# Performance work log

Measured on AMD Instinct MI355X. Metric: run time of the kernel, lower is better.

## Reference

```python
import jax, jax.numpy as jnp
import numpy as np

N_BASIS = 1024
KERNEL_SIZE = 1024
STRIDE = 256
N_BINS = N_BASIS // 2 + 1  # 513 (onesided)


def setup_inputs() -> dict:
    key = jax.random.key(0)
    x = jax.random.normal(key, (16, 1, 524288), dtype=jnp.float32)
    # omega = 2*pi*arange(n_basis//2+1)/n_basis (as in __init__)
    frequency = (2.0 * np.pi * jnp.arange(N_BINS, dtype=jnp.float32) / N_BASIS)
    # periodic hann window, matching torch.hann_window default
    n = jnp.arange(KERNEL_SIZE, dtype=jnp.float32)
    window = 0.5 * (1.0 - jnp.cos(2.0 * np.pi * n / KERNEL_SIZE))
    return {"x": x, "frequency": frequency, "window": window}


def _conv1d(x, kernel, stride):
    # x: (B, 1, T), kernel: (O, K) -> (B, O, F)
    return jax.lax.conv_general_dilated(
        x, kernel[:, None, :], window_strides=(stride,), padding="VALID",
        dimension_numbers=("NCH", "OIH", "NCH"))


def reference(x, frequency, window):
    # Fourier basis: cos(-omega*n), sin(-omega*n), windowed
    n = jnp.arange(KERNEL_SIZE, dtype=x.dtype)
    omega_n = frequency[:, None] * n[None, :]          # (513, K)
    basis_real = jnp.cos(-omega_n) * window            # (513, K)
    basis_imag = jnp.sin(-omega_n) * window            # (513, K)
    out_real = _conv1d(x, basis_real, STRIDE)          # (B, 513, F)
    out_imag = _conv1d(x, basis_imag, STRIDE)          # (B, 513, F)
    # return_complex=False: permute(0,3,1,2).view -> [real; imag] stacked on channels
    return jnp.concatenate([out_real, out_imag], axis=1)  # (B, 1026, F)
```

## Files before the change

### kernel.cpp

```cpp
#include <hip/hip_runtime.h>
#include <hip/hip_bf16.h>

#define TLEN   524288
#define NBATCH 16
#define KSZ    1024
#define NBINS  513
#define NCH    1026
#define NFRM   2045
#define HOP    256
#define MROWS  1024
#define KS2    512
#define NFPAD  2048
#define BM 128
#define BN 128
#define BK 64
#define NT 8
#define PREP_BASIS_BLKS 2048
#define PREP_FOLD_BLKS  8192

typedef __bf16 bf16x8 __attribute__((ext_vector_type(8)));
typedef float  f32x4  __attribute__((ext_vector_type(4)));
typedef unsigned short us8 __attribute__((ext_vector_type(8)));

__device__ __forceinline__ unsigned short f2b(float f) {
    return __builtin_bit_cast(unsigned short, __float2bfloat16(f));
}

__global__ void prep_k(const float* __restrict__ x,
                       const float* __restrict__ window,
                       __hip_bfloat16* __restrict__ basis,
                       __hip_bfloat16* __restrict__ u,
                       __hip_bfloat16* __restrict__ v,
                       float* __restrict__ out) {
    if (blockIdx.x < PREP_BASIS_BLKS) {
        int idx = blockIdx.x * 256 + threadIdx.x;
        int g = idx >> 9;
        int k = idx & (KS2 - 1);
        float val = 0.0f;
        if (g < 512) {
            if (k == 0) val = (g & 1) ? -1.0f : 1.0f;
            else {
                int m = (g * k) & (KSZ - 1);
                val = window[k] *
                      cosf((float)m * (6.283185307179586f / (float)KSZ));
            }
        } else if (g < 1023) {
            if (k != 0) {
                int c = g - 511;
                int m = (c * k) & (KSZ - 1);
                val = -window[k] *
                      sinf((float)m * (6.283185307179586f / (float)KSZ));
            }
        }
        basis[idx] = __float2bfloat16(val);
        return;
    }
    int idx = (blockIdx.x - PREP_BASIS_BLKS) * 256 + threadIdx.x;
    int b = idx >> 17;
    int rem = idx & ((1 << 17) - 1);
    int f = rem >> 6;
    int c = rem & 63;
    size_t orow = ((size_t)b * NFPAD + f) * KS2 + c * 8;
    us8 uo = {0, 0, 0, 0, 0, 0, 0, 0};
    us8 vo = {0, 0, 0, 0, 0, 0, 0, 0};
    float nacc = 0.0f;
    if (f < NFRM) {
        const float* xp = x + (size_t)b * TLEN + (size_t)f * HOP;
        float4 fw0 = *(const float4*)(xp + c * 8);
        float4 fw1 = *(const float4*)(xp + c * 8 + 4);
        float4 m0  = *(const float4*)(xp + 1016 - c * 8);
        float4 m1  = *(const float4*)(xp + 1020 - c * 8);
        float fwv[8] = {fw0.x, fw0.y, fw0.z, fw0.w,
                        fw1.x, fw1.y, fw1.z, fw1.w};
        float mv[9];
        mv[0] = m0.x; mv[1] = m0.y; mv[2] = m0.z; mv[3] = m0.w;
        mv[4] = m1.x; mv[5] = m1.y; mv[6] = m1.z; mv[7] = m1.w;
        mv[8] = (c > 0) ? xp[1024 - c * 8] : 0.0f;
        #pragma unroll
        for (int e = 0; e < 8; ++e) {
            float xf = fwv[e];
            float xm = mv[8 - e];
            float uval = xf + xm;
            uo[e] = f2b(uval);
            vo[e] = f2b(xf - xm);
            float wk = window[c * 8 + e];
            nacc += ((e & 1) ? -wk : wk) * uval;
        }
        if (c == 0) {
            float x512 = xp[512];
            uo[0] = f2b(x512);
            vo[0] = 0;
            nacc += x512;
        }
    }
    *(us8*)((unsigned short*)u + orow) = uo;
    *(us8*)((unsigned short*)v + orow) = vo;
    #pragma unroll
    for (int o = 32; o > 0; o >>= 1) nacc += __shfl_xor(nacc, o);
    if (f < NFRM) {
        if (c == 0) out[((size_t)b * NCH + 512) * NFRM + f] = nacc;
        if (c == 1) out[((size_t)b * NCH + 513) * NFRM + f] = 0.0f;
    }
}

__launch_bounds__(256, 2)
__global__ void stft_gemm_k(const __hip_bfloat16* __restrict__ basis,
                            const __hip_bfloat16* __restrict__ u,
                            const __hip_bfloat16* __restrict__ v,
                            float* __restrict__ out) {
    __shared__ __hip_bfloat16 As[BM * BK];
    __shared__ __hip_bfloat16 Bs[BN * BK];

    const int tid  = threadIdx.x;
    const int wave = tid >> 6;
    const int lane = tid & 63;
    const int l16  = lane & 15;
    const int lg   = lane >> 4;
    const int wr   = wave >> 1;
    const int wc   = wave & 1;
    const int f0   = blockIdx.x * BN;
    const int c0   = blockIdx.y * BM;
    const int bb   = blockIdx.z;
    const bool isV = (c0 >= 512);
    const __hip_bfloat16* Bmat =
        (isV ? v : u) + (size_t)bb * NFPAD * KS2;

    f32x4 acc[4][4] = {};

    for (int kt = 0; kt < NT; ++kt) {
        const int k0 = kt * BK;
        #pragma unroll
        for (int it = 0; it < 4; ++it) {
            int flat = it * 256 + tid;
            int row  = flat >> 3;
            int ch   = flat & 7;
            int kch  = ch ^ (row & 7);
            const __hip_bfloat16* sa =
                basis + (size_t)(c0 + row) * KS2 + k0 + kch * 8;
            __builtin_amdgcn_global_load_lds(
                (const __attribute__((address_space(1))) void*)sa,
                (__attribute__((address_space(3))) void*)
                    ((char*)As + (it * 256 + wave * 64) * 16),
                16, 0, 0);
            const __hip_bfloat16* sb =
                Bmat + (size_t)(f0 + row) * KS2 + k0 + kch * 8;
            __builtin_amdgcn_global_load_lds(
                (const __attribute__((address_space(1))) void*)sb,
                (__attribute__((address_space(3))) void*)
                    ((char*)Bs + (it * 256 + wave * 64) * 16),
                16, 0, 0);
        }
        __syncthreads();

        #pragma unroll
        for (int ks = 0; ks < 2; ++ks) {
            bf16x8 a[4], b[4];
            #pragma unroll
            for (int m = 0; m < 4; ++m) {
                int row  = wr * 64 + m * 16 + l16;
                int slot = row * 8 + ((ks * 4 + lg) ^ (row & 7));
                a[m] = *(const bf16x8*)((const char*)As + slot * 16);
            }
            #pragma unroll
            for (int n = 0; n < 4; ++n) {
                int row  = wc * 64 + n * 16 + l16;
                int slot = row * 8 + ((ks * 4 + lg) ^ (row & 7));
                b[n] = *(const bf16x8*)((const char*)Bs + slot * 16);
            }
            #pragma unroll
            for (int m = 0; m < 4; ++m)
                #pragma unroll
                for (int n = 0; n < 4; ++n)
                    acc[m][n] = __builtin_amdgcn_mfma_f32_16x16x32_bf16(
                        a[m], b[n], acc[m][n], 0, 0, 0);
        }
        __syncthreads();
    }

    const int choff = isV ? 2 : 0;
    float* outb = out + (size_t)bb * NCH * NFRM;
    #pragma unroll
    for (int m = 0; m < 4; ++m) {
        int g0 = c0 + wr * 64 + m * 16 + lg * 4;
        #pragma unroll
        for (int n = 0; n < 4; ++n) {
            int f = f0 + wc * 64 + n * 16 + l16;
            if (f < NFRM) {
                #pragma unroll
                for (int i = 0; i < 4; ++i)
                    outb[(size_t)(g0 + i + choff) * NFRM + f] = acc[m][n][i];
            }
        }
    }
}

extern "C" void kernel_launch(void* const* d_in, const int* in_sizes, int n_in,
                              void* d_out, int out_size, void* d_ws, size_t ws_size,
                              hipStream_t stream) {
    const float* x      = (const float*)d_in[0];
    const float* window = (const float*)d_in[2];

    __hip_bfloat16* basis = (__hip_bfloat16*)d_ws;
    __hip_bfloat16* ub = (__hip_bfloat16*)((char*)d_ws + (size_t)MROWS * KS2 * 2);
    __hip_bfloat16* vb = ub + (size_t)NBATCH * NFPAD * KS2;
    float* outp = (float*)d_out;

    prep_k<<<PREP_BASIS_BLKS + PREP_FOLD_BLKS, 256, 0, stream>>>(
        x, window, basis, ub, vb, outp);

    dim3 grid(NFPAD / BN, MROWS / BM, NBATCH);
    stft_gemm_k<<<grid, 256, 0, stream>>>(basis, ub, vb, outp);
}
```

Before: 72.54 us.

## Apply second-level even/odd frequency folding to halve GEMM reduction depth

Adds a further symmetry fold of each windowed frame: the 1024-tap window is split into quarter segments, and even/odd frequency bins get separate 256-deep basis planes, so the GEMM K dimension drops from 512 to 256. The prep kernel now applies the window to the input and writes four folded planes plus an x[512] side array. The GEMM epilogue scatters results to interleaved output channels with special-case corrections. This cuts MFMA work in half at the cost of a more complex prep, strided interleaved output writes, and extra bf16 rounding of windowed sums.

```diff
diff --git a/kernel.cpp b/kernel.cpp
--- a/kernel.cpp
+++ b/kernel.cpp
@@ -8,14 +8,15 @@
 #define NCH    1026
 #define NFRM   2045
 #define HOP    256
-#define MROWS  1024
-#define KS2    512
 #define NFPAD  2048
+#define KF     256
+#define M2     1024
+#define PS ((size_t)NBATCH * NFPAD * KF)
 #define BM 128
 #define BN 128
 #define BK 64
-#define NT 8
-#define PREP_BASIS_BLKS 2048
+#define NT 4
+#define PREP_BASIS_BLKS 1024
 #define PREP_FOLD_BLKS  8192
 
 typedef __bf16 bf16x8 __attribute__((ext_vector_type(8)));
@@ -29,84 +30,121 @@
 __global__ void prep_k(const float* __restrict__ x,
                        const float* __restrict__ window,
                        __hip_bfloat16* __restrict__ basis,
-                       __hip_bfloat16* __restrict__ u,
-                       __hip_bfloat16* __restrict__ v,
+                       __hip_bfloat16* __restrict__ planes,
+                       float* __restrict__ x512a,
                        float* __restrict__ out) {
     if (blockIdx.x < PREP_BASIS_BLKS) {
         int idx = blockIdx.x * 256 + threadIdx.x;
-        int g = idx >> 9;
-        int k = idx & (KS2 - 1);
+        int g = idx >> 8;
+        int k = idx & 255;
         float val = 0.0f;
-        if (g < 512) {
+        if (g < 256) {
             if (k == 0) val = (g & 1) ? -1.0f : 1.0f;
-            else {
-                int m = (g * k) & (KSZ - 1);
-                val = window[k] *
-                      cosf((float)m * (6.283185307179586f / (float)KSZ));
-            }
-        } else if (g < 1023) {
-            if (k != 0) {
-                int c = g - 511;
-                int m = (c * k) & (KSZ - 1);
-                val = -window[k] *
-                      sinf((float)m * (6.283185307179586f / (float)KSZ));
-            }
+            else { int m = (g * k) & 511;
+                   val = cosf((float)m * (6.283185307179586f / 512.0f)); }
+        } else if (g < 512) {
+            int d = g - 256, c = 2 * d + 1;
+            if (k) { int m = (c * k) & 1023;
+                     val = cosf((float)m * (6.283185307179586f / 1024.0f)); }
+        } else if (g < 768) {
+            int d = g - 512;
+            if (d <= 254 && k) {
+                int c = 2 * d + 2, m = (c * k) & 1023;
+                val = -sinf((float)m * (6.283185307179586f / 1024.0f));
+            }
+        } else {
+            int d = g - 768, c = 2 * d + 1;
+            if (k == 0) val = (d & 1) ? 1.0f : -1.0f;
+            else { int m = (c * k) & 1023;
+                   val = -sinf((float)m * (6.283185307179586f / 1024.0f)); }
         }
         basis[idx] = __float2bfloat16(val);
         return;
     }
-    int idx = (blockIdx.x - PREP_BASIS_BLKS) * 256 + threadIdx.x;
-    int b = idx >> 17;
-    int rem = idx & ((1 << 17) - 1);
-    int f = rem >> 6;
-    int c = rem & 63;
-    size_t orow = ((size_t)b * NFPAD + f) * KS2 + c * 8;
-    us8 uo = {0, 0, 0, 0, 0, 0, 0, 0};
-    us8 vo = {0, 0, 0, 0, 0, 0, 0, 0};
-    float nacc = 0.0f;
+    int wid  = (blockIdx.x - PREP_BASIS_BLKS) * 4 + (threadIdx.x >> 6);
+    int lane = threadIdx.x & 63;
+    int b = wid >> 11;
+    int f = wid & 2047;
+    int isQ = lane >> 5;
+    int j   = lane & 31;
+    size_t off = ((size_t)b * NFPAD + f) * KF + j * 8;
+    unsigned short* P0 = (unsigned short*)planes + (isQ ? 2 * PS : 0) + off;
+    unsigned short* P1 = (unsigned short*)planes + (isQ ? 3 * PS : PS) + off;
+    us8 o0 = {0, 0, 0, 0, 0, 0, 0, 0};
+    us8 o1 = {0, 0, 0, 0, 0, 0, 0, 0};
+    float nacc = 0.0f, x512 = 0.0f;
     if (f < NFRM) {
         const float* xp = x + (size_t)b * TLEN + (size_t)f * HOP;
-        float4 fw0 = *(const float4*)(xp + c * 8);
-        float4 fw1 = *(const float4*)(xp + c * 8 + 4);
-        float4 m0  = *(const float4*)(xp + 1016 - c * 8);
-        float4 m1  = *(const float4*)(xp + 1020 - c * 8);
-        float fwv[8] = {fw0.x, fw0.y, fw0.z, fw0.w,
-                        fw1.x, fw1.y, fw1.z, fw1.w};
-        float mv[9];
-        mv[0] = m0.x; mv[1] = m0.y; mv[2] = m0.z; mv[3] = m0.w;
-        mv[4] = m1.x; mv[5] = m1.y; mv[6] = m1.z; mv[7] = m1.w;
-        mv[8] = (c > 0) ? xp[1024 - c * 8] : 0.0f;
+        float4 a0 = *(const float4*)(xp + j * 8);
+        float4 a1 = *(const float4*)(xp + j * 8 + 4);
+        float4 r0 = *(const float4*)(xp + 1016 - j * 8);
+        float4 r1 = *(const float4*)(xp + 1020 - j * 8);
+        float4 cc0 = *(const float4*)(xp + 504 - j * 8);
+        float4 cc1 = *(const float4*)(xp + 508 - j * 8);
+        float4 d0 = *(const float4*)(xp + 512 + j * 8);
+        float4 d1 = *(const float4*)(xp + 512 + j * 8 + 4);
+        float4 w0 = *(const float4*)(window + j * 8);
+        float4 w1 = *(const float4*)(window + j * 8 + 4);
+        float4 wb0 = *(const float4*)(window + 504 - j * 8);
+        float4 wb1 = *(const float4*)(window + 508 - j * 8);
+        float S1 = (j > 0) ? xp[1024 - j * 8] : 0.0f;
+        float S2 = xp[512 - j * 8];
+        float SW = window[512 - j * 8];
+        float Av[8] = {a0.x, a0.y, a0.z, a0.w, a1.x, a1.y, a1.z, a1.w};
+        float Rv[8] = {r0.x, r0.y, r0.z, r0.w, r1.x, r1.y, r1.z, r1.w};
+        float Cv[8] = {cc0.x, cc0.y, cc0.z, cc0.w, cc1.x, cc1.y, cc1.z, cc1.w};
+        float Dv[8] = {d0.x, d0.y, d0.z, d0.w, d1.x, d1.y, d1.z, d1.w};
+        float Wa[8] = {w0.x, w0.y, w0.z, w0.w, w1.x, w1.y, w1.z, w1.w};
+        float Wb[8] = {wb0.x, wb0.y, wb0.z, wb0.w, wb1.x, wb1.y, wb1.z, wb1.w};
+        float p0slot = 0.0f;
         #pragma unroll
         for (int e = 0; e < 8; ++e) {
-            float xf = fwv[e];
-            float xm = mv[8 - e];
-            float uval = xf + xm;
-            uo[e] = f2b(uval);
-            vo[e] = f2b(xf - xm);
-            float wk = window[c * 8 + e];
-            nacc += ((e & 1) ? -wk : wk) * uval;
-        }
-        if (c == 0) {
-            float x512 = xp[512];
-            uo[0] = f2b(x512);
-            vo[0] = 0;
-            nacc += x512;
-        }
-    }
-    *(us8*)((unsigned short*)u + orow) = uo;
-    *(us8*)((unsigned short*)v + orow) = vo;
+            float xm1 = (e == 0) ? S1 : Rv[8 - e];
+            float xm2 = (e == 0) ? S2 : Cv[8 - e];
+            float wkb = (e == 0) ? SW : Wb[8 - e];
+            float u1 = Av[e] + xm1, v1 = Av[e] - xm1;
+            float u2 = xm2 + Dv[e], v2 = xm2 - Dv[e];
+            float t1 = Wa[e] * u1, t2 = wkb * u2;
+            float s1 = Wa[e] * v1, s2 = wkb * v2;
+            if (!isQ) {
+                float pp = t1 + t2;
+                o0[e] = f2b(pp);
+                o1[e] = f2b(t1 - t2);
+                if (e == 0) p0slot = pp;
+                else nacc += (e & 1) ? -pp : pp;
+            } else {
+                o0[e] = f2b(s1 - s2);
+                o1[e] = f2b(s1 + s2);
+            }
+        }
+        if (j == 0) {
+            float w256 = window[256], xa = xp[256], xc = xp[768];
+            if (!isQ) { float wu256 = w256 * (xa + xc);
+                        o0[0] = f2b(wu256); o1[0] = 0; p0slot = wu256; }
+            else      { float wv256 = w256 * (xa - xc);
+                        o0[0] = 0; o1[0] = f2b(wv256); }
+        }
+        if (!isQ) nacc += p0slot;
+        x512 = xp[512];
+    }
+    *(us8*)P0 = o0;
+    *(us8*)P1 = o1;
     #pragma unroll
     for (int o = 32; o > 0; o >>= 1) nacc += __shfl_xor(nacc, o);
     if (f < NFRM) {
-        if (c == 0) out[((size_t)b * NCH + 512) * NFRM + f] = nacc;
-        if (c == 1) out[((size_t)b * NCH + 513) * NFRM + f] = 0.0f;
+        if (lane == 0) {
+            x512a[b * NFPAD + f] = x512;
+            out[((size_t)b * NCH + 512) * NFRM + f] = x512 + nacc;
+        }
+        if (lane == 1) out[((size_t)b * NCH + 513) * NFRM + f] = 0.0f;
+        if (lane == 2) out[((size_t)b * NCH + 1025) * NFRM + f] = 0.0f;
     }
 }
 
 __launch_bounds__(256, 2)
 __global__ void stft_gemm_k(const __hip_bfloat16* __restrict__ basis,
-                            const __hip_bfloat16* __restrict__ u,
-                            const __hip_bfloat16* __restrict__ v,
+                            const __hip_bfloat16* __restrict__ planes,
+                            const float* __restrict__ x512a,
                             float* __restrict__ out) {
     __shared__ __hip_bfloat16 As[BM * BK];
     __shared__ __hip_bfloat16 Bs[BN * BK];
@@ -121,9 +159,9 @@
     const int f0   = blockIdx.x * BN;
     const int c0   = blockIdx.y * BM;
     const int bb   = blockIdx.z;
-    const bool isV = (c0 >= 512);
+    const int cls  = blockIdx.y >> 1;
     const __hip_bfloat16* Bmat =
-        (isV ? v : u) + (size_t)bb * NFPAD * KS2;
+        planes + (size_t)cls * PS + (size_t)bb * NFPAD * KF;
 
     f32x4 acc[4][4] = {};
 
@@ -136,14 +174,14 @@
             int ch   = flat & 7;
             int kch  = ch ^ (row & 7);
             const __hip_bfloat16* sa =
-                basis + (size_t)(c0 + row) * KS2 + k0 + kch * 8;
+                basis + (size_t)(c0 + row) * KF + k0 + kch * 8;
             __builtin_amdgcn_global_load_lds(
                 (const __attribute__((address_space(1))) void*)sa,
                 (__attribute__((address_space(3))) void*)
                     ((char*)As + (it * 256 + wave * 64) * 16),
                 16, 0, 0);
             const __hip_bfloat16* sb =
-                Bmat + (size_t)(f0 + row) * KS2 + k0 + kch * 8;
+                Bmat + (size_t)(f0 + row) * KF + k0 + kch * 8;
             __builtin_amdgcn_global_load_lds(
                 (const __attribute__((address_space(1))) void*)sb,
                 (__attribute__((address_space(3))) void*)
@@ -177,7 +215,9 @@
         __syncthreads();
     }
 
-    const int choff = isV ? 2 : 0;
+    const int chA  = (cls == 0) ? 0 : (cls == 1) ? 1 : (cls == 2) ? 515 : 514;
+    const int dmax = (cls == 2) ? 254 : 255;
+    const float* xv = x512a + bb * NFPAD;
     float* outb = out + (size_t)bb * NCH * NFRM;
     #pragma unroll
     for (int m = 0; m < 4; ++m) {
@@ -186,9 +226,14 @@
         for (int n = 0; n < 4; ++n) {
             int f = f0 + wc * 64 + n * 16 + l16;
             if (f < NFRM) {
+                float xadd = (cls == 0) ? xv[f] : (cls == 1) ? -xv[f] : 0.0f;
                 #pragma unroll
-                for (int i = 0; i < 4; ++i)
-                    outb[(size_t)(g0 + i + choff) * NFRM + f] = acc[m][n][i];
+                for (int i = 0; i < 4; ++i) {
+                    int d = g0 + i - cls * 256;
+                    if (d <= dmax)
+                        outb[(size_t)(chA + 2 * d) * NFRM + f] =
+                            acc[m][n][i] + xadd;
+                }
             }
         }
     }
@@ -200,14 +245,14 @@
     const float* x      = (const float*)d_in[0];
     const float* window = (const float*)d_in[2];
 
-    __hip_bfloat16* basis = (__hip_bfloat16*)d_ws;
-    __hip_bfloat16* ub = (__hip_bfloat16*)((char*)d_ws + (size_t)MROWS * KS2 * 2);
-    __hip_bfloat16* vb = ub + (size_t)NBATCH * NFPAD * KS2;
+    __hip_bfloat16* basis  = (__hip_bfloat16*)d_ws;
+    __hip_bfloat16* planes = basis + (size_t)M2 * KF;
+    float*          x512a  = (float*)(planes + 4 * PS);
     float* outp = (float*)d_out;
 
     prep_k<<<PREP_BASIS_BLKS + PREP_FOLD_BLKS, 256, 0, stream>>>(
-        x, window, basis, ub, vb, outp);
-
-    dim3 grid(NFPAD / BN, MROWS / BM, NBATCH);
-    stft_gemm_k<<<grid, 256, 0, stream>>>(basis, ub, vb, outp);
-}
+        x, window, basis, planes, x512a, outp);
+
+    dim3 grid(NFPAD / BN, M2 / BM, NBATCH);
+    stft_gemm_k<<<grid, 256, 0, stream>>>(basis, planes, x512a, outp);
+}
```

Result: slower. 85.27 us (+17.6%).
